# Kernel tuning notes

Measured on AMD Instinct MI355X. Metric: run time of the kernel, lower is better.

## Reference

```python
import jax, jax.numpy as jnp
import numpy as np

N_COLS = 4096
N_ROWS = 4096
H = 64          # args.hidden1
S = 2           # per-edge supp feature count (cv_supp/vc_supp dim 0)
S_VO = 2        # vo_supp feature dim
S_CO = 2        # co_supp feature dim
EDGE_DENSITY = 0.03


def setup_inputs() -> dict:
    key = jax.random.key(0)
    ks = jax.random.split(key, 20)
    col_hidden = jax.random.normal(ks[0], (N_COLS, H), jnp.float32)
    row_hidden = jax.random.normal(ks[1], (N_ROWS, H), jnp.float32)
    obj_hidden = jax.random.normal(ks[2], (1, H), jnp.float32)
    # sparse bipartite adjacency encoded in supp[0] != 0 (as in the TF code)
    mask = jax.random.bernoulli(ks[3], EDGE_DENSITY, (N_ROWS, N_COLS))
    cv_supp = jax.random.normal(ks[4], (S, N_ROWS, N_COLS), jnp.float32) * mask[None]
    vc_supp = jnp.transpose(cv_supp, (0, 2, 1))  # [S, ncols, nrows]
    vo_supp = jax.random.normal(ks[5], (N_COLS, S_VO), jnp.float32)
    co_supp = jax.random.normal(ks[6], (N_ROWS, S_CO), jnp.float32)
    w = 0.05
    W_vo = jax.random.normal(ks[7], (2 * H, H), jnp.float32) * w
    W_oc = jax.random.normal(ks[8], (2 * H, H), jnp.float32) * w
    W_vc = jax.random.normal(ks[9], (2 * H, H), jnp.float32) * w
    W_co = jax.random.normal(ks[10], (2 * H, H), jnp.float32) * w
    W_ov = jax.random.normal(ks[11], (2 * H, H), jnp.float32) * w
    W_cv = jax.random.normal(ks[12], (2 * H, H), jnp.float32) * w
    # attention scorer nets: Dense(concat_dim -> 1) + sigmoid
    w_attn_vo = jax.random.normal(ks[13], (2 * H + S_VO, 1), jnp.float32) * 0.1
    b_attn_vo = jnp.zeros((), jnp.float32)
    w_attn_co = jax.random.normal(ks[14], (2 * H + S_CO, 1), jnp.float32) * 0.1
    b_attn_co = jnp.zeros((), jnp.float32)
    # pairwise attn nets decomposed into [col | supp | row] weight slices
    w_cv_col = jax.random.normal(ks[15], (H,), jnp.float32) * 0.1
    w_cv_supp = jax.random.normal(ks[16], (S,), jnp.float32) * 0.1
    w_cv_row = jax.random.normal(ks[17], (H,), jnp.float32) * 0.1
    b_cv = jnp.zeros((), jnp.float32)
    w_vc_row = jax.random.normal(ks[18], (H,), jnp.float32) * 0.1
    w_vc_supp = jax.random.normal(ks[19], (S,), jnp.float32) * 0.1
    w_vc_col = jax.random.normal(jax.random.fold_in(key, 99), (H,), jnp.float32) * 0.1
    b_vc = jnp.zeros((), jnp.float32)
    return dict(col_hidden=col_hidden, row_hidden=row_hidden, obj_hidden=obj_hidden,
                cv_supp=cv_supp, vc_supp=vc_supp, vo_supp=vo_supp, co_supp=co_supp,
                W_vo=W_vo, W_oc=W_oc, W_vc=W_vc, W_co=W_co, W_ov=W_ov, W_cv=W_cv,
                w_attn_vo=w_attn_vo, b_attn_vo=b_attn_vo,
                w_attn_co=w_attn_co, b_attn_co=b_attn_co,
                w_cv_col=w_cv_col, w_cv_supp=w_cv_supp, w_cv_row=w_cv_row, b_cv=b_cv,
                w_vc_row=w_vc_row, w_vc_supp=w_vc_supp, w_vc_col=w_vc_col, b_vc=b_vc)


def _forward(col_hidden, row_hidden, obj_hidden, cv_supp, vc_supp, vo_supp, co_supp,
             W_vo, W_oc, W_vc, W_co, W_ov, W_cv,
             w_attn_vo, b_attn_vo, w_attn_co, b_attn_co,
             w_cv_col, w_cv_supp, w_cv_row, b_cv,
             w_vc_row, w_vc_supp, w_vc_col, b_vc):
    act = jax.nn.relu
    ncols, nrows = col_hidden.shape[0], row_hidden.shape[0]
    # ---- v -> o: attend over all columns, update obj node ----
    vo_in = jnp.concatenate([col_hidden, vo_supp,
                             jnp.broadcast_to(obj_hidden, (ncols, H))], axis=1)
    a_vo = jax.nn.sigmoid(vo_in @ w_attn_vo + b_attn_vo)          # [ncols, 1]
    v_o_out = a_vo.T @ col_hidden                                  # [1, H]
    obj = act(jnp.concatenate([obj_hidden, v_o_out], axis=1) @ W_vo)
    # ---- v -> c: per-row ragged neighbor attention, vectorized via masked pairwise scores ----
    nbr_cv = cv_supp[0] != 0                                       # [nrows, ncols]
    logits_cv = ((row_hidden @ w_cv_row)[:, None]
                 + (col_hidden @ w_cv_col)[None, :]
                 + jnp.einsum('snc,s->nc', cv_supp, w_cv_supp) + b_cv)
    score_cv = jnp.where(nbr_cv, jax.nn.sigmoid(logits_cv), 0.0)   # [nrows, ncols]
    v_out = score_cv @ col_hidden                                  # [nrows, H]
    o_c_out = act(jnp.concatenate([jnp.broadcast_to(obj, (nrows, H)), row_hidden], axis=1) @ W_oc)
    row_next = act(jnp.concatenate([o_c_out, v_out], axis=1) @ W_vc)
    # ---- c -> o ----
    co_in = jnp.concatenate([row_next, co_supp,
                             jnp.broadcast_to(obj, (nrows, H))], axis=1)
    a_co = jax.nn.sigmoid(co_in @ w_attn_co + b_attn_co)           # [nrows, 1]
    c_o_out = a_co.T @ row_next                                    # [1, H]
    obj = act(jnp.concatenate([obj, c_o_out], axis=1) @ W_co)
    # ---- c -> v ----
    nbr_vc = vc_supp[0] != 0                                       # [ncols, nrows]
    logits_vc = ((col_hidden @ w_vc_col)[:, None]
                 + (row_next @ w_vc_row)[None, :]
                 + jnp.einsum('scn,s->cn', vc_supp, w_vc_supp) + b_vc)
    score_vc = jnp.where(nbr_vc, jax.nn.sigmoid(logits_vc), 0.0)   # [ncols, nrows]
    c_out = score_vc @ row_next                                    # [ncols, H]
    o_v_out = act(jnp.concatenate([jnp.broadcast_to(obj, (ncols, H)), col_hidden], axis=1) @ W_ov)
    col_next = act(jnp.concatenate([o_v_out, c_out], axis=1) @ W_cv)
    return col_next, row_next, obj


def reference(col_hidden, row_hidden, obj_hidden, cv_supp, vc_supp, vo_supp, co_supp,
              W_vo, W_oc, W_vc, W_co, W_ov, W_cv,
              w_attn_vo, b_attn_vo, w_attn_co, b_attn_co,
              w_cv_col, w_cv_supp, w_cv_row, b_cv,
              w_vc_row, w_vc_supp, w_vc_col, b_vc):
    col_next, row_next, obj = _forward(
        col_hidden, row_hidden, obj_hidden, cv_supp, vc_supp, vo_supp, co_supp,
        W_vo, W_oc, W_vc, W_co, W_ov, W_cv,
        w_attn_vo, b_attn_vo, w_attn_co, b_attn_co,
        w_cv_col, w_cv_supp, w_cv_row, b_cv,
        w_vc_row, w_vc_supp, w_vc_col, b_vc)
    # original layer also passes the supp tensors through unchanged
    return (col_next, row_next, obj, cv_supp, vc_supp, vo_supp, co_supp)
```

## Files before the change

### kernel.cpp

```cpp
#include <hip/hip_runtime.h>
#include <math.h>

typedef float f4 __attribute__((ext_vector_type(4)));

#define PLANE (4096*4096)

#define OUT_COL 0
#define OUT_ROW 262144
#define OUT_OBJ 524288
#define OUT_CV  524352
#define OUT_VC  34078784
#define OUT_VO  67633216
#define OUT_CO  67641408

#define WS_VO_P 0
#define WS_CO_P 4096
#define WS_OBJ1 8192
#define WS_RDCV 8256
#define WS_CDCV 12352
#define WS_RDVC 16448
#define WS_CDVC 20544
#define WS_PART 24640

__device__ __forceinline__ float sigf(float x) {
    return 1.0f / (1.0f + __expf(-x));
}

__device__ __forceinline__ float enc_sj(float s, int j) {
    return __uint_as_float((__float_as_uint(s) & 0xFFFFF000u) | (unsigned)j);
}

__device__ __forceinline__ void attn_body64(
    int blk, int t, const float* __restrict__ X, const float* __restrict__ supp,
    const float* __restrict__ obj, const float* __restrict__ wat,
    const float* __restrict__ bat, float* __restrict__ accP,
    const float* __restrict__ wextra, float* __restrict__ dextra,
    float* sA, float* sAcc)
{
    const int w = t >> 6, lane = t & 63;
    if (t < 64) {
        const int i = blk * 64 + t;
        float od = 0.f;
        for (int h = 0; h < 64; ++h) od += obj[h] * wat[66 + h];
        float x = bat[0] + od + supp[i*2] * wat[64] + supp[i*2+1] * wat[65];
        const f4* Xr = (const f4*)(X + i*64);
        f4 xd = 0.f, dd = 0.f;
        #pragma unroll
        for (int q = 0; q < 16; ++q) {
            f4 xv = Xr[q];
            xd += xv * ((const f4*)wat)[q];
            if (wextra) dd += xv * ((const f4*)wextra)[q];
        }
        x += xd.x + xd.y + xd.z + xd.w;
        if (dextra) dextra[i] = dd.x + dd.y + dd.z + dd.w;
        sA[t] = sigf(x);
        sAcc[t] = 0.f;
    }
    __syncthreads();
    float partial = 0.f;
    const int jbase = blk * 64 + w * 16;
    for (int j = 0; j < 16; ++j)
        partial += sA[w*16 + j] * X[(jbase + j)*64 + lane];
    atomicAdd(&sAcc[lane], partial);
    __syncthreads();
    if (t < 64) accP[blk*64 + t] = sAcc[t];
}

__global__ __launch_bounds__(256) void k_front(
    const float* __restrict__ col_hidden, const float* __restrict__ row_hidden,
    const float* __restrict__ w_cv_col, const float* __restrict__ w_vc_col,
    const float* __restrict__ w_cv_row,
    float* __restrict__ cdcv, float* __restrict__ cdvc, float* __restrict__ rdcv,
    const float* __restrict__ vo_supp, const float* __restrict__ co_supp,
    float* __restrict__ out_vo, float* __restrict__ out_co,
    const float* __restrict__ obj_hidden, const float* __restrict__ w_attn_vo,
    const float* __restrict__ b_attn_vo, float* __restrict__ voP)
{
    __shared__ float sA[64];
    __shared__ float sAcc[64];
    const int t = threadIdx.x;
    if (blockIdx.x < 3072) {
        const int gw = blockIdx.x * 4 + (t >> 6);
        const int lane = t & 63;
        const int which = gw >> 12;
        const int row = gw & 4095;
        const float* x; const float* w; float* dst;
        if (which == 0)      { x = col_hidden; w = w_cv_col; dst = cdcv; }
        else if (which == 1) { x = col_hidden; w = w_vc_col; dst = cdvc; }
        else                 { x = row_hidden; w = w_cv_row; dst = rdcv; }
        float v = x[row * 64 + lane] * w[lane];
        #pragma unroll
        for (int off = 32; off; off >>= 1) v += __shfl_down(v, off, 64);
        if (lane == 0) dst[row] = v;
        return;
    }
    if (blockIdx.x < 3088) {
        const int idx = (blockIdx.x - 3072) * 256 + t;
        if (idx < 2048) ((f4*)out_vo)[idx] = ((const f4*)vo_supp)[idx];
        else            ((f4*)out_co)[idx - 2048] = ((const f4*)co_supp)[idx - 2048];
        return;
    }
    attn_body64(blockIdx.x - 3088, t, col_hidden, vo_supp, obj_hidden,
                w_attn_vo, b_attn_vo, voP, nullptr, nullptr, sA, sAcc);
}

__global__ __launch_bounds__(256) void k_attn(
    const float* __restrict__ X, const float* __restrict__ supp,
    const float* __restrict__ obj, const float* __restrict__ wat,
    const float* __restrict__ bat, float* __restrict__ accP,
    const float* __restrict__ wextra, float* __restrict__ dextra)
{
    __shared__ float sA[64];
    __shared__ float sAcc[64];
    attn_body64(blockIdx.x, threadIdx.x, X, supp, obj, wat, bat, accP,
                wextra, dextra, sA, sAcc);
}

__global__ __launch_bounds__(256, 4) void k_score(
    const float* __restrict__ supp0c, const float* __restrict__ supp1c,
    const float* __restrict__ Bm,
    const float* __restrict__ rdot, const float* __restrict__ cdot,
    const float* __restrict__ wsup, const float* __restrict__ bias,
    float* __restrict__ vout,
    const float* __restrict__ objL, const float* __restrict__ objRp,
    const float* __restrict__ Wobj, float* __restrict__ objDst)
{
    __shared__ __align__(16) float list[4][16][32];
    const int t = threadIdx.x;

    if (blockIdx.x == 1024) {
        float* red = &list[0][0][0];
        if (t < 64) {
            float r = 0.f;
            for (int b = 0; b < 64; ++b) r += objRp[b*64 + t];
            red[t] = r;
        }
        __syncthreads();
        if (t < 64) {
            float acc = 0.f;
            for (int k = 0; k < 64; ++k) acc += objL[k] * Wobj[k*64 + t];
            for (int k = 0; k < 64; ++k) acc += red[k] * Wobj[(64+k)*64 + t];
            objDst[t] = fmaxf(acc, 0.f);
        }
        return;
    }

    const int w = t >> 6, lane = t & 63;
    const int r = blockIdx.x * 4 + w;
    const float w0 = wsup[0], w1 = wsup[1], bv = bias[0];
    const float rd = rdot[r];

    #pragma unroll 4
    for (int c = 0; c < 16; ++c) {
        const size_t g = (size_t)r * 4096 + c * 256 + lane * 4;
        f4 a0 = *(const f4*)(supp0c + g);
        f4 a1 = *(const f4*)(supp1c + g);
        const f4 cd = *(const f4*)(cdot + c * 256 + lane * 4);
        f4 lg = rd + cd + w0 * a0 + w1 * a1 + bv;
        const int c0 = (a0.x != 0.f), c1 = (a0.y != 0.f);
        const int c2 = (a0.z != 0.f), c3 = (a0.w != 0.f);
        const int m = c0 + c1 + c2 + c3;
        int sum = m;
        #pragma unroll
        for (int d = 1; d < 64; d <<= 1) {
            int x = __shfl_up(sum, d, 64);
            if (lane >= d) sum += x;
        }
        int pos = sum - m;
        float* L = &list[w][c][0];
        const int jb = c * 256 + lane * 4;
        if (c0) { if (pos < 31) L[pos] = enc_sj(sigf(lg.x), jb + 0); ++pos; }
        if (c1) { if (pos < 31) L[pos] = enc_sj(sigf(lg.y), jb + 1); ++pos; }
        if (c2) { if (pos < 31) L[pos] = enc_sj(sigf(lg.z), jb + 2); ++pos; }
        if (c3) { if (pos < 31) L[pos] = enc_sj(sigf(lg.w), jb + 3); ++pos; }
        if (lane == 63) L[31] = __int_as_float(sum < 31 ? sum : 31);
    }
    asm volatile("s_waitcnt lgkmcnt(0)" ::: "memory");
    __builtin_amdgcn_sched_barrier(0);

    float acc = 0.f;
    for (int c = 0; c < 16; ++c) {
        const float* L = &list[w][c][0];
        const int n = __float_as_int(L[31]);
        for (int k = 0; k < n; ++k) {
            const unsigned u = __float_as_uint(L[k]);
            const int j = (int)(u & 0xFFFu);
            const float s = __uint_as_float(u & 0xFFFFF000u);
            acc += s * Bm[(size_t)j * 64 + lane];
        }
    }
    vout[(size_t)r * 64 + lane] = acc;
}

__global__ __launch_bounds__(256) void k_mlp2(
    const float* __restrict__ objx, const float* __restrict__ base,
    const float* __restrict__ W1, const float* __restrict__ part,
    const float* __restrict__ W2, float* __restrict__ dst)
{
    __shared__ float mid[4][64];
    __shared__ float accs[4][64];
    const int t = threadIdx.x, w = t >> 6, h = t & 63;
    const int n = blockIdx.x * 4 + w;
    accs[w][h] = part[(size_t)n * 64 + h];
    float m = 0.f;
    for (int k = 0; k < 64; ++k) m += objx[k] * W1[k*64 + h];
    for (int k = 0; k < 64; ++k) m += base[n*64 + k] * W1[(64+k)*64 + h];
    mid[w][h] = fmaxf(m, 0.f);
    __syncthreads();
    float o = 0.f;
    for (int k = 0; k < 64; ++k) o += mid[w][k] * W2[k*64 + h];
    for (int k = 0; k < 64; ++k) o += accs[w][k] * W2[(64+k)*64 + h];
    dst[n*64 + h] = fmaxf(o, 0.f);
}

extern "C" void kernel_launch(void* const* d_in, const int* in_sizes, int n_in,
                              void* d_out, int out_size, void* d_ws, size_t ws_size,
                              hipStream_t stream)
{
    const float* col_hidden = (const float*)d_in[0];
    const float* row_hidden = (const float*)d_in[1];
    const float* obj_hidden = (const float*)d_in[2];
    const float* cv_supp    = (const float*)d_in[3];
    const float* vc_supp    = (const float*)d_in[4];
    const float* vo_supp    = (const float*)d_in[5];
    const float* co_supp    = (const float*)d_in[6];
    const float* W_vo       = (const float*)d_in[7];
    const float* W_oc       = (const float*)d_in[8];
    const float* W_vc       = (const float*)d_in[9];
    const float* W_co       = (const float*)d_in[10];
    const float* W_ov       = (const float*)d_in[11];
    const float* W_cv       = (const float*)d_in[12];
    const float* w_attn_vo  = (const float*)d_in[13];
    const float* b_attn_vo  = (const float*)d_in[14];
    const float* w_attn_co  = (const float*)d_in[15];
    const float* b_attn_co  = (const float*)d_in[16];
    const float* w_cv_col   = (const float*)d_in[17];
    const float* w_cv_supp  = (const float*)d_in[18];
    const float* w_cv_row   = (const float*)d_in[19];
    const float* b_cv       = (const float*)d_in[20];
    const float* w_vc_row   = (const float*)d_in[21];
    const float* w_vc_supp  = (const float*)d_in[22];
    const float* w_vc_col   = (const float*)d_in[23];
    const float* b_vc       = (const float*)d_in[24];

    float* out = (float*)d_out;
    float* ws  = (float*)d_ws;
    const size_t SUPP_BYTES = (size_t)2 * PLANE * sizeof(float);

    k_front<<<3152, 256, 0, stream>>>(col_hidden, row_hidden, w_cv_col, w_vc_col, w_cv_row,
                                      ws + WS_CDCV, ws + WS_CDVC, ws + WS_RDCV,
                                      vo_supp, co_supp, out + OUT_VO, out + OUT_CO,
                                      obj_hidden, w_attn_vo, b_attn_vo, ws + WS_VO_P);
    k_score<<<1025, 256, 0, stream>>>(cv_supp, cv_supp + PLANE, col_hidden,
                                      ws + WS_RDCV, ws + WS_CDCV, w_cv_supp, b_cv,
                                      ws + WS_PART,
                                      obj_hidden, ws + WS_VO_P, W_vo, ws + WS_OBJ1);
    hipMemcpyAsync(out + OUT_CV, cv_supp, SUPP_BYTES, hipMemcpyDeviceToDevice, stream);
    k_mlp2<<<1024, 256, 0, stream>>>(ws + WS_OBJ1, row_hidden, W_oc, ws + WS_PART, W_vc,
                                     out + OUT_ROW);
    k_attn<<<64, 256, 0, stream>>>(out + OUT_ROW, co_supp, ws + WS_OBJ1, w_attn_co, b_attn_co,
                                   ws + WS_CO_P, w_vc_row, ws + WS_RDVC);
    k_score<<<1025, 256, 0, stream>>>(vc_supp, vc_supp + PLANE, out + OUT_ROW,
                                      ws + WS_CDVC, ws + WS_RDVC, w_vc_supp, b_vc,
                                      ws + WS_PART,
                                      ws + WS_OBJ1, ws + WS_CO_P, W_co, out + OUT_OBJ);
    hipMemcpyAsync(out + OUT_VC, vc_supp, SUPP_BYTES, hipMemcpyDeviceToDevice, stream);
    k_mlp2<<<1024, 256, 0, stream>>>(out + OUT_OBJ, col_hidden, W_ov, ws + WS_PART, W_cv,
                                     out + OUT_COL);
}
```

Baseline: 599.3 us.

## Fuse supp passthrough copy into score kernel and skip all-zero chunks

The separate device-to-device memcpy of each supp tensor is replaced by having the score kernel write its loaded supp vectors directly to the output, so the 128MB passthrough no longer requires a second full read. The score loop is split into a first pass that loads, copies and records a per-lane nonzero bitmask, and a second pass that reloads supp and cdot only for chunks with nonzeros. The reload relies on the data still being in cache, and the kernel now carries heavy store traffic, which may lower the overlap with compute.

```diff
diff --git a/kernel.cpp b/kernel.cpp
--- a/kernel.cpp
+++ b/kernel.cpp
@@ -116,12 +116,12 @@
                 wextra, dextra, sA, sAcc);
 }
 
-__global__ __launch_bounds__(256, 4) void k_score(
-    const float* __restrict__ supp0c, const float* __restrict__ supp1c,
+__global__ __launch_bounds__(256, 4) void k_big(
+    const float* __restrict__ supp0, const float* __restrict__ supp1,
     const float* __restrict__ Bm,
     const float* __restrict__ rdot, const float* __restrict__ cdot,
     const float* __restrict__ wsup, const float* __restrict__ bias,
-    float* __restrict__ vout,
+    float* __restrict__ vout, float* __restrict__ pass0, float* __restrict__ pass1,
     const float* __restrict__ objL, const float* __restrict__ objRp,
     const float* __restrict__ Wobj, float* __restrict__ objDst)
 {
@@ -149,16 +149,34 @@
     const int r = blockIdx.x * 4 + w;
     const float w0 = wsup[0], w1 = wsup[1], bv = bias[0];
     const float rd = rdot[r];
-
+    const size_t rowg = (size_t)r * 4096;
+
+    unsigned mymask = 0;
     #pragma unroll 4
     for (int c = 0; c < 16; ++c) {
-        const size_t g = (size_t)r * 4096 + c * 256 + lane * 4;
-        f4 a0 = *(const f4*)(supp0c + g);
-        f4 a1 = *(const f4*)(supp1c + g);
-        const f4 cd = *(const f4*)(cdot + c * 256 + lane * 4);
-        f4 lg = rd + cd + w0 * a0 + w1 * a1 + bv;
-        const int c0 = (a0.x != 0.f), c1 = (a0.y != 0.f);
-        const int c2 = (a0.z != 0.f), c3 = (a0.w != 0.f);
+        const size_t g = rowg + c * 256 + lane * 4;
+        f4 a0 = *(const f4*)(supp0 + g);
+        f4 a1 = *(const f4*)(supp1 + g);
+        *(f4*)(pass0 + g) = a0;
+        *(f4*)(pass1 + g) = a1;
+        const unsigned nz = (unsigned)((a0.x != 0.f) | (a0.y != 0.f) |
+                                       (a0.z != 0.f) | (a0.w != 0.f));
+        mymask |= nz << c;
+    }
+
+    for (int c = 0; c < 16; ++c) {
+        const int nzme = (mymask >> c) & 1;
+        int c0 = 0, c1 = 0, c2 = 0, c3 = 0;
+        f4 lg = 0.f;
+        if (nzme) {
+            const size_t g = rowg + c * 256 + lane * 4;
+            f4 a0 = *(const f4*)(supp0 + g);
+            f4 a1 = *(const f4*)(supp1 + g);
+            const f4 cd = *(const f4*)(cdot + c * 256 + lane * 4);
+            lg = rd + cd + w0 * a0 + w1 * a1 + bv;
+            c0 = (a0.x != 0.f); c1 = (a0.y != 0.f);
+            c2 = (a0.z != 0.f); c3 = (a0.w != 0.f);
+        }
         const int m = c0 + c1 + c2 + c3;
         int sum = m;
         #pragma unroll
@@ -189,7 +207,7 @@
             acc += s * Bm[(size_t)j * 64 + lane];
         }
     }
-    vout[(size_t)r * 64 + lane] = acc;
+    vout[rowg / 64 + lane] = acc;
 }
 
 __global__ __launch_bounds__(256) void k_mlp2(
@@ -245,26 +263,23 @@
 
     float* out = (float*)d_out;
     float* ws  = (float*)d_ws;
-    const size_t SUPP_BYTES = (size_t)2 * PLANE * sizeof(float);
 
     k_front<<<3152, 256, 0, stream>>>(col_hidden, row_hidden, w_cv_col, w_vc_col, w_cv_row,
                                       ws + WS_CDCV, ws + WS_CDVC, ws + WS_RDCV,
                                       vo_supp, co_supp, out + OUT_VO, out + OUT_CO,
                                       obj_hidden, w_attn_vo, b_attn_vo, ws + WS_VO_P);
-    k_score<<<1025, 256, 0, stream>>>(cv_supp, cv_supp + PLANE, col_hidden,
-                                      ws + WS_RDCV, ws + WS_CDCV, w_cv_supp, b_cv,
-                                      ws + WS_PART,
-                                      obj_hidden, ws + WS_VO_P, W_vo, ws + WS_OBJ1);
-    hipMemcpyAsync(out + OUT_CV, cv_supp, SUPP_BYTES, hipMemcpyDeviceToDevice, stream);
+    k_big<<<1025, 256, 0, stream>>>(cv_supp, cv_supp + PLANE, col_hidden,
+                                    ws + WS_RDCV, ws + WS_CDCV, w_cv_supp, b_cv,
+                                    ws + WS_PART, out + OUT_CV, out + OUT_CV + PLANE,
+                                    obj_hidden, ws + WS_VO_P, W_vo, ws + WS_OBJ1);
     k_mlp2<<<1024, 256, 0, stream>>>(ws + WS_OBJ1, row_hidden, W_oc, ws + WS_PART, W_vc,
                                      out + OUT_ROW);
     k_attn<<<64, 256, 0, stream>>>(out + OUT_ROW, co_supp, ws + WS_OBJ1, w_attn_co, b_attn_co,
                                    ws + WS_CO_P, w_vc_row, ws + WS_RDVC);
-    k_score<<<1025, 256, 0, stream>>>(vc_supp, vc_supp + PLANE, out + OUT_ROW,
-                                      ws + WS_CDVC, ws + WS_RDVC, w_vc_supp, b_vc,
-                                      ws + WS_PART,
-                                      ws + WS_OBJ1, ws + WS_CO_P, W_co, out + OUT_OBJ);
-    hipMemcpyAsync(out + OUT_VC, vc_supp, SUPP_BYTES, hipMemcpyDeviceToDevice, stream);
+    k_big<<<1025, 256, 0, stream>>>(vc_supp, vc_supp + PLANE, out + OUT_ROW,
+                                    ws + WS_CDVC, ws + WS_RDVC, w_vc_supp, b_vc,
+                                    ws + WS_PART, out + OUT_VC, out + OUT_VC + PLANE,
+                                    ws + WS_OBJ1, ws + WS_CO_P, W_co, out + OUT_OBJ);
     k_mlp2<<<1024, 256, 0, stream>>>(out + OUT_OBJ, col_hidden, W_ov, ws + WS_PART, W_cv,
                                      out + OUT_COL);
 }
```

New measurement: 592.8 us. About the same (-1.1%).
